# Kernel tuning notes

Measured on AMD Instinct MI355X. Metric: run time of the kernel, lower is better.

The kernel has to match this reference:

```python
import jax, jax.numpy as jnp
import numpy as np

B, S, H, NH = 2, 2048, 2048, 32
HD = H // NH  # 64

def _causal_mask(b, s, dtype=jnp.float32):
    neg = jnp.finfo(dtype).min
    m = jnp.where(jnp.tril(jnp.ones((s, s), dtype=bool)), 0.0, neg).astype(dtype)
    return jnp.broadcast_to(m[None, None], (b, 1, s, s))

def setup_inputs() -> dict:
    key = jax.random.key(0)
    k1, k2, k3, k4, k5 = jax.random.split(key, 5)
    scale = 1.0 / np.sqrt(H)
    return {
        "hidden_states": jax.random.normal(k1, (B, S, H), jnp.float32),
        "attention_mask": _causal_mask(B, S),
        "Wq": jax.random.normal(k2, (H, H), jnp.float32) * scale,
        "Wk": jax.random.normal(k3, (H, H), jnp.float32) * scale,
        "Wv": jax.random.normal(k4, (H, H), jnp.float32) * scale,
        "Wo": jax.random.normal(k5, (H, H), jnp.float32) * scale,
    }

def reference(hidden_states, attention_mask, Wq, Wk, Wv, Wo):
    b, s, _ = hidden_states.shape
    dt = hidden_states.dtype
    def proj(W):  # torch Linear: x @ W.T -> [b, nh, s, hd]
        return (hidden_states @ W.T).reshape(b, s, NH, HD).transpose(0, 2, 1, 3)
    q, k, v = proj(Wq), proj(Wk), proj(Wv)
    attn = jnp.einsum('bhqd,bhkd->bhqk', q, k) / np.sqrt(HD)
    attn = attn + attention_mask
    attn = jnp.maximum(attn, jnp.finfo(attn.dtype).min)
    attn = jax.nn.softmax(attn.astype(jnp.float32), axis=-1).astype(dt)
    out = jnp.einsum('bhqk,bhkd->bhqd', attn, v)
    out = out.transpose(0, 2, 1, 3).reshape(b, s, H)
    return out @ Wo.T
```

## Files before the change

### kernel.cpp

```cpp
#include <hip/hip_runtime.h>
#include <hip/hip_bf16.h>
#include <stdint.h>

#define S_LEN 2048
#define NHEAD 32
#define HDIM  64

using bf16x8 = __attribute__((ext_vector_type(8))) short;
using f32x4  = __attribute__((ext_vector_type(4))) float;

__device__ __forceinline__ uint16_t f2bf(float f) {
  union { float f; uint32_t u; } c; c.f = f;
  uint32_t u = c.u;
  return (uint16_t)((u + 0x7FFFu + ((u >> 16) & 1u)) >> 16);
}

__device__ __forceinline__ void load_lds16(const void* g, void* l) {
  __builtin_amdgcn_global_load_lds(
      (const __attribute__((address_space(1))) void*)g,
      (__attribute__((address_space(3))) void*)l, 16, 0, 0);
}

__global__ __launch_bounds__(256) void conv_f32_bf16(
    const float* __restrict__ in, uint16_t* __restrict__ out, int n4) {
  int i = blockIdx.x * 256 + threadIdx.x;
  if (i < n4) {
    float4 v = ((const float4*)in)[i];
    uint16_t o0 = f2bf(v.x), o1 = f2bf(v.y), o2 = f2bf(v.z), o3 = f2bf(v.w);
    uint64_t packed = (uint64_t)o0 | ((uint64_t)o1 << 16) |
                      ((uint64_t)o2 << 32) | ((uint64_t)o3 << 48);
    ((uint64_t*)out)[i] = packed;
  }
}

__global__ __launch_bounds__(512, 2) void gemm_qk(
    const uint16_t* __restrict__ A, const uint16_t* __restrict__ Bw,
    uint16_t* __restrict__ Qo, uint16_t* __restrict__ Ko, float qscale) {
  extern __shared__ char smem[];
  const int t = threadIdx.x;
  const int lane = t & 63, w = t >> 6;
  const int lrow = lane & 15, lgrp = lane >> 4;
  const int wr = w >> 2, wc = w & 3;
  const int id = blockIdx.x;
  const int swz = (id & 7) * 32 + (id >> 3);
  const int bm = (swz & 15) * 256, bn = (swz >> 4) * 256;
  constexpr int NT = 2048 / 32;

  const f32x4 zero4 = {0.f, 0.f, 0.f, 0.f};
  f32x4 acc[8][4];
#pragma unroll
  for (int mi = 0; mi < 8; ++mi)
#pragma unroll
    for (int ni = 0; ni < 4; ++ni) acc[mi][ni] = zero4;

  auto stage_mat = [&](const uint16_t* __restrict__ G, int grow0,
                       char* ldsbase, int kt) {
#pragma unroll
    for (int j = 0; j < 2; ++j) {
      const int s = t + j * 512;
      const int row = s >> 2;
      const int sc = (s & 3) ^ ((row >> 1) & 3);
      load_lds16(G + (size_t)(grow0 + row) * 2048 + kt + sc * 8,
                 ldsbase + j * 8192 + w * 1024);
    }
  };
  auto lda = [&](const char* Ab, int mi) -> bf16x8 {
    const int row = wr * 128 + mi * 16 + lrow;
    return *(const bf16x8*)(Ab + row * 64 + ((lgrp ^ ((row >> 1) & 3)) << 4));
  };
  auto ldb = [&](const char* Bb, int ni) -> bf16x8 {
    const int row = wc * 64 + ni * 16 + lrow;
    return *(const bf16x8*)(Bb + row * 64 + ((lgrp ^ ((row >> 1) & 3)) << 4));
  };

  stage_mat(A, bm, smem, 0);
  stage_mat(Bw, bn, smem + 16384, 0);
  stage_mat(A, bm, smem + 32768, 32);
  stage_mat(Bw, bn, smem + 32768 + 16384, 32);
  asm volatile("s_waitcnt vmcnt(4)" ::: "memory");
  __builtin_amdgcn_s_barrier();

  for (int kt = 0; kt < NT; ++kt) {
    char* cur = smem + (kt % 3) * 32768;
    char* nx2 = smem + ((kt + 2) % 3) * 32768;
    const int kg = (kt + 2) * 32;
    bf16x8 aF[4], bF[4];

    if (kt + 2 < NT) stage_mat(A, bm, nx2, kg);
#pragma unroll
    for (int mi = 0; mi < 4; ++mi) aF[mi] = lda(cur, mi);
#pragma unroll
    for (int ni = 0; ni < 4; ++ni) bF[ni] = ldb(cur + 16384, ni);
    __builtin_amdgcn_s_barrier();
    asm volatile("s_waitcnt lgkmcnt(0)" ::: "memory");
    __builtin_amdgcn_sched_barrier(0);
    __builtin_amdgcn_s_setprio(1);
#pragma unroll
    for (int mi = 0; mi < 4; ++mi)
#pragma unroll
      for (int ni = 0; ni < 4; ++ni)
        acc[mi][ni] = __builtin_amdgcn_mfma_f32_16x16x32_bf16(
            aF[mi], bF[ni], acc[mi][ni], 0, 0, 0);
    __builtin_amdgcn_s_setprio(0);
    __builtin_amdgcn_s_barrier();

    if (kt + 2 < NT) stage_mat(Bw, bn, nx2 + 16384, kg);
#pragma unroll
    for (int mi = 0; mi < 4; ++mi) aF[mi] = lda(cur, 4 + mi);
    __builtin_amdgcn_s_barrier();
    asm volatile("s_waitcnt lgkmcnt(0)" ::: "memory");
    __builtin_amdgcn_sched_barrier(0);
    __builtin_amdgcn_s_setprio(1);
#pragma unroll
    for (int mi = 0; mi < 4; ++mi)
#pragma unroll
      for (int ni = 0; ni < 4; ++ni)
        acc[4 + mi][ni] = __builtin_amdgcn_mfma_f32_16x16x32_bf16(
            aF[mi], bF[ni], acc[4 + mi][ni], 0, 0, 0);
    __builtin_amdgcn_s_setprio(0);
    if (kt < NT - 2) {
      asm volatile("s_waitcnt vmcnt(4)" ::: "memory");
    } else {
      asm volatile("s_waitcnt vmcnt(0)" ::: "memory");
    }
    __builtin_amdgcn_s_barrier();
  }

  const bool isQ = (bn < 2048);
#pragma unroll
  for (int mi = 0; mi < 8; ++mi) {
#pragma unroll
    for (int ni = 0; ni < 4; ++ni) {
      const int n = bn + wc * 64 + ni * 16 + lrow;
      const int n2 = isQ ? n : (n - 2048);
      const int h = n2 >> 6, d = n2 & 63;
#pragma unroll
      for (int r = 0; r < 4; ++r) {
        const int m = bm + wr * 128 + mi * 16 + lgrp * 4 + r;
        const int b = m >> 11, s = m & 2047;
        const size_t off = (((size_t)(b * NHEAD + h) * S_LEN + s) * HDIM) + d;
        if (isQ) Qo[off] = f2bf(acc[mi][ni][r] * qscale);
        else     Ko[off] = f2bf(acc[mi][ni][r]);
      }
    }
  }
}

template<int MODE>
__global__ __launch_bounds__(256) void gemm_nt(
    const uint16_t* __restrict__ A, const uint16_t* __restrict__ B,
    void* __restrict__ C, int M, int N, int K, float scale) {
  constexpr int BK = 64;
  __shared__ __align__(16) uint16_t As[128 * BK];
  __shared__ __align__(16) uint16_t Bs[128 * BK];

  const int t = threadIdx.x;
  const int lane = t & 63, w = t >> 6;
  const int lrow = lane & 15, lgrp = lane >> 4;
  const int bm = blockIdx.y * 128, bn = blockIdx.x * 128;
  const int wm = (w >> 1) * 64, wn = (w & 1) * 64;

  const f32x4 zero4 = {0.f, 0.f, 0.f, 0.f};
  f32x4 acc[4][4];
#pragma unroll
  for (int mi = 0; mi < 4; ++mi)
#pragma unroll
    for (int ni = 0; ni < 4; ++ni) acc[mi][ni] = zero4;

  const int rowS = t >> 3;
  const int chunk = t & 7;
  const int srcChunk = chunk ^ (rowS & 7);

  for (int kt = 0; kt < K; kt += BK) {
    __syncthreads();
#pragma unroll
    for (int it = 0; it < 4; ++it) {
      const int r = it * 32 + rowS;
      load_lds16(A + (size_t)(bm + r) * K + kt + srcChunk * 8,
                 (char*)As + it * 4096 + w * 1024);
      load_lds16(B + (size_t)(bn + r) * K + kt + srcChunk * 8,
                 (char*)Bs + it * 4096 + w * 1024);
    }
    __syncthreads();

#pragma unroll
    for (int ks = 0; ks < 2; ++ks) {
      bf16x8 af[4], bf[4];
#pragma unroll
      for (int mi = 0; mi < 4; ++mi) {
        const int ra = wm + mi * 16 + lrow;
        const int cb = ks * 4 + lgrp;
        af[mi] = *(const bf16x8*)((const char*)As +
                                  ra * 128 + ((cb ^ (ra & 7)) * 16));
        const int rb = wn + mi * 16 + lrow;
        bf[mi] = *(const bf16x8*)((const char*)Bs +
                                  rb * 128 + ((cb ^ (rb & 7)) * 16));
      }
#pragma unroll
      for (int mi = 0; mi < 4; ++mi)
#pragma unroll
        for (int ni = 0; ni < 4; ++ni)
          acc[mi][ni] = __builtin_amdgcn_mfma_f32_16x16x32_bf16(
              af[mi], bf[ni], acc[mi][ni], 0, 0, 0);
    }
  }

#pragma unroll
  for (int mi = 0; mi < 4; ++mi) {
#pragma unroll
    for (int ni = 0; ni < 4; ++ni) {
      const int n = bn + wn + ni * 16 + lrow;
#pragma unroll
      for (int r = 0; r < 4; ++r) {
        const int m = bm + wm + mi * 16 + lgrp * 4 + r;
        const float v = acc[mi][ni][r] * scale;
        if (MODE == 2) {
          ((float*)C)[(size_t)m * N + n] = v;
        } else {
          const int h = m >> 6, d = m & 63;
          const int b = n >> 11, s = n & 2047;
          ((uint16_t*)C)[(((size_t)(b * NHEAD + h) * HDIM + d) * S_LEN) + s] =
              f2bf(v);
        }
      }
    }
  }
}

__global__ __launch_bounds__(256, 4) void attn_kernel(
    const uint16_t* __restrict__ Q, const uint16_t* __restrict__ K,
    const uint16_t* __restrict__ Vt, uint16_t* __restrict__ O) {
  __shared__ __align__(16) uint16_t Ks[2][64 * 64];
  __shared__ __align__(16) uint16_t Vs[2][64 * 64];
  __shared__ __align__(16) uint16_t Ps[4][16 * 64];

  const int t = threadIdx.x, lane = t & 63, w = t >> 6;
  const int lrow = lane & 15, lgrp = lane >> 4;
  const int id = blockIdx.x;
  const int bh = (id & 7) | (((id >> 3) & 7) << 3);
  const int pair = id >> 6;
  const int b = bh >> 5, h = bh & 31;

  const uint16_t* Qbh = Q + (size_t)bh * S_LEN * HDIM;
  const uint16_t* Kbh = K + (size_t)bh * S_LEN * HDIM;
  const uint16_t* Vbh = Vt + (size_t)bh * HDIM * S_LEN;

  const int srow = lane >> 3;
  const int schunk = (lane & 7) ^ srow;

  const f32x4 zero4 = {0.f, 0.f, 0.f, 0.f};
  const int xk = lrow & 7;

  auto stage = [&](int k0, int bi) {
#pragma unroll
    for (int i = 0; i < 2; ++i) {
      const int r = i * 32 + w * 8 + srow;
      load_lds16(Kbh + (size_t)(k0 + r) * HDIM + schunk * 8,
                 (char*)&Ks[bi][0] + i * 4096 + w * 1024);
      load_lds16(Vbh + (size_t)r * S_LEN + k0 + schunk * 8,
                 (char*)&Vs[bi][0] + i * 4096 + w * 1024);
    }
  };

  for (int pass = 0; pass < 2; ++pass) {
    const int qt = pass ? (31 - pair) : pair;
    const int qbase = qt * 64 + w * 16;

    bf16x8 qf0, qf1;
    {
      const uint16_t* qp = Qbh + (size_t)(qbase + lrow) * HDIM + lgrp * 8;
      qf0 = *(const bf16x8*)qp;
      qf1 = *(const bf16x8*)(qp + 32);
    }
    f32x4 oacc[4] = {zero4, zero4, zero4, zero4};
    float lsum[4] = {0.f, 0.f, 0.f, 0.f};

    auto pstore = [&](int tt, int r, float p) {
      const int q = lgrp * 4 + r;
      const int c = (2 * tt + (lrow >> 3)) ^ (q & 7);
      Ps[w][q * 64 + c * 8 + (lrow & 7)] = f2bf(p);
    };

    for (int kt = 0; kt <= qt; ++kt) {
      const int cur = kt & 1;
      if (kt == 0) {
        __syncthreads();
        stage(0, 0);
      }
      __syncthreads();
      if (kt < qt) stage((kt + 1) * 64, cur ^ 1);

      const char* Kc = (const char*)&Ks[cur][0];
      const char* Vc = (const char*)&Vs[cur][0];
      const int k0 = kt * 64;

      auto qk_chunk = [&](int tt) -> f32x4 {
        const char* base = Kc + (tt * 16 + lrow) * 128;
        bf16x8 kf0 = *(const bf16x8*)(base + ((lgrp ^ xk) << 4));
        bf16x8 kf1 = *(const bf16x8*)(base + (((4 + lgrp) ^ xk) << 4));
        f32x4 s = __builtin_amdgcn_mfma_f32_16x16x32_bf16(qf0, kf0, zero4, 0, 0, 0);
        return __builtin_amdgcn_mfma_f32_16x16x32_bf16(qf1, kf1, s, 0, 0, 0);
      };

      if (kt < qt) {
        f32x4 sacc[4];
        __builtin_amdgcn_s_setprio(1);
#pragma unroll
        for (int tt = 0; tt < 4; ++tt) sacc[tt] = qk_chunk(tt);
        __builtin_amdgcn_s_setprio(0);
#pragma unroll
        for (int tt = 0; tt < 4; ++tt)
#pragma unroll
          for (int r = 0; r < 4; ++r) {
            const float p = __expf(sacc[tt][r]);
            lsum[r] += p;
            pstore(tt, r, p);
          }
      } else {
        for (int tt = 0; tt < 4; ++tt) {
          if (tt <= w) {
            const f32x4 s = qk_chunk(tt);
            const int kk = k0 + tt * 16 + lrow;
#pragma unroll
            for (int r = 0; r < 4; ++r) {
              const int qg = qbase + lgrp * 4 + r;
              const float p = (kk <= qg) ? __expf(s[r]) : 0.f;
              lsum[r] += p;
              pstore(tt, r, p);
            }
          } else {
#pragma unroll
            for (int r = 0; r < 4; ++r) pstore(tt, r, 0.f);
          }
        }
      }

      __builtin_amdgcn_s_setprio(1);
#pragma unroll
      for (int s = 0; s < 2; ++s) {
        const int cs = ((s << 2) + lgrp) ^ xk;
        bf16x8 pf = *(const bf16x8*)((const char*)&Ps[w][0] +
                                     lrow * 128 + (cs << 4));
#pragma unroll
        for (int dt = 0; dt < 4; ++dt) {
          bf16x8 vf = *(const bf16x8*)(Vc + (dt * 16 + lrow) * 128 + (cs << 4));
          oacc[dt] = __builtin_amdgcn_mfma_f32_16x16x32_bf16(pf, vf, oacc[dt],
                                                             0, 0, 0);
        }
      }
      __builtin_amdgcn_s_setprio(0);
    }

#pragma unroll
    for (int off = 1; off <= 8; off <<= 1)
#pragma unroll
      for (int r = 0; r < 4; ++r) lsum[r] += __shfl_xor(lsum[r], off, 64);

#pragma unroll
    for (int r = 0; r < 4; ++r) {
      const float inv = 1.0f / lsum[r];
      const int qg = qbase + lgrp * 4 + r;
#pragma unroll
      for (int dt = 0; dt < 4; ++dt)
        O[((size_t)b * S_LEN + qg) * 2048 + h * 64 + dt * 16 + lrow] =
            f2bf(oacc[dt][r] * inv);
    }
  }
}

extern "C" void kernel_launch(void* const* d_in, const int* in_sizes, int n_in,
                              void* d_out, int out_size, void* d_ws,
                              size_t ws_size, hipStream_t stream) {
  const float* X  = (const float*)d_in[0];
  const float* Wq = (const float*)d_in[2];
  const float* Wk = (const float*)d_in[3];
  const float* Wv = (const float*)d_in[4];
  const float* Wo = (const float*)d_in[5];
  float* out = (float*)d_out;

  char* ws = (char*)d_ws;
  uint16_t* Xbf = (uint16_t*)ws;
  uint16_t* Wqk = (uint16_t*)(ws + 16777216);
  uint16_t* Qb  = (uint16_t*)(ws + 33554432);
  uint16_t* Kb  = (uint16_t*)(ws + 50331648);
  uint16_t* Wsm = (uint16_t*)(ws + 67108864);
  uint16_t* Vtb = Wqk;
  uint16_t* Ob  = Xbf;

  const float qscale = 0.125f;

  hipFuncSetAttribute((const void*)gemm_qk,
                      hipFuncAttributeMaxDynamicSharedMemorySize, 98304);

  conv_f32_bf16<<<8192, 256, 0, stream>>>(X, Xbf, 2097152);
  conv_f32_bf16<<<4096, 256, 0, stream>>>(Wq, Wqk, 1048576);
  conv_f32_bf16<<<4096, 256, 0, stream>>>(Wk, Wqk + 4194304, 1048576);
  gemm_qk<<<256, 512, 98304, stream>>>(Xbf, Wqk, Qb, Kb, qscale);
  conv_f32_bf16<<<4096, 256, 0, stream>>>(Wv, Wsm, 1048576);
  gemm_nt<1><<<dim3(32, 16), 256, 0, stream>>>(Wsm, Xbf, Vtb, 2048, 4096, 2048, 1.0f);
  attn_kernel<<<dim3(1024), 256, 0, stream>>>(Qb, Kb, Vtb, Ob);
  conv_f32_bf16<<<4096, 256, 0, stream>>>(Wo, Wsm, 1048576);
  gemm_nt<2><<<dim3(16, 32), 256, 0, stream>>>(Ob, Wsm, out, 4096, 2048, 2048, 1.0f);
}
```

Before: 246.6 us.

## Rewrite attention with 32x32 MFMA, register-resident P, and batch input conversions

The attention kernel now gives each wave 32 query rows and uses 32x32x16 bf16 MFMAs. The S^T layout lets exponentiated scores be packed with v_cvt_pk_bf16_f32 and permlane32 swaps straight into A-operands, so the per-wave LDS round trip for P goes away. The grid is halved to 128-row query tiles with causal pairing and the occupancy hint drops to 3 blocks per SM. The X/Wq/Wk/Wv f32-to-bf16 conversions are merged into one launch, adding branchy source selection per thread and more register pressure in attention.

```diff
diff --git a/kernel.cpp b/kernel.cpp
--- a/kernel.cpp
+++ b/kernel.cpp
@@ -8,6 +8,7 @@
 
 using bf16x8 = __attribute__((ext_vector_type(8))) short;
 using f32x4  = __attribute__((ext_vector_type(4))) float;
+using f32x16 = __attribute__((ext_vector_type(16))) float;
 
 __device__ __forceinline__ uint16_t f2bf(float f) {
   union { float f; uint32_t u; } c; c.f = f;
@@ -19,6 +20,36 @@
   __builtin_amdgcn_global_load_lds(
       (const __attribute__((address_space(1))) void*)g,
       (__attribute__((address_space(3))) void*)l, 16, 0, 0);
+}
+
+__device__ __forceinline__ f32x16 mfma32(bf16x8 a, bf16x8 b, f32x16 c) {
+  return __builtin_amdgcn_mfma_f32_32x32x16_bf16(a, b, c, 0, 0, 0);
+}
+
+__device__ __forceinline__ uint32_t cvtpk(float lo, float hi_) {
+  uint32_t d;
+  asm("v_cvt_pk_bf16_f32 %0, %1, %2" : "=v"(d) : "v"(lo), "v"(hi_));
+  return d;
+}
+__device__ __forceinline__ void plswap(uint32_t& a, uint32_t& b) {
+  asm volatile("v_permlane32_swap_b32 %0, %1" : "+v"(a), "+v"(b));
+}
+
+__global__ __launch_bounds__(256) void conv_batch(
+    const float* __restrict__ X, const float* __restrict__ Wq,
+    const float* __restrict__ Wk, const float* __restrict__ Wv,
+    uint16_t* __restrict__ Xbf, uint16_t* __restrict__ Wqk,
+    uint16_t* __restrict__ Wvb) {
+  int i = blockIdx.x * 256 + threadIdx.x;
+  const float* src; uint16_t* dst; int o;
+  if (i < 2097152)      { src = X;  dst = Xbf;           o = i; }
+  else if (i < 3145728) { src = Wq; dst = Wqk;           o = i - 2097152; }
+  else if (i < 4194304) { src = Wk; dst = Wqk + 4194304; o = i - 3145728; }
+  else                  { src = Wv; dst = Wvb;           o = i - 4194304; }
+  float4 v = ((const float4*)src)[o];
+  uint64_t packed = (uint64_t)f2bf(v.x) | ((uint64_t)f2bf(v.y) << 16) |
+                    ((uint64_t)f2bf(v.z) << 32) | ((uint64_t)f2bf(v.w) << 48);
+  ((uint64_t*)dst)[o] = packed;
 }
 
 __global__ __launch_bounds__(256) void conv_f32_bf16(
@@ -26,9 +57,8 @@
   int i = blockIdx.x * 256 + threadIdx.x;
   if (i < n4) {
     float4 v = ((const float4*)in)[i];
-    uint16_t o0 = f2bf(v.x), o1 = f2bf(v.y), o2 = f2bf(v.z), o3 = f2bf(v.w);
-    uint64_t packed = (uint64_t)o0 | ((uint64_t)o1 << 16) |
-                      ((uint64_t)o2 << 32) | ((uint64_t)o3 << 48);
+    uint64_t packed = (uint64_t)f2bf(v.x) | ((uint64_t)f2bf(v.y) << 16) |
+                      ((uint64_t)f2bf(v.z) << 32) | ((uint64_t)f2bf(v.w) << 48);
     ((uint64_t*)out)[i] = packed;
   }
 }
@@ -227,18 +257,18 @@
   }
 }
 
-__global__ __launch_bounds__(256, 4) void attn_kernel(
+__global__ __launch_bounds__(256, 3) void attn_kernel(
     const uint16_t* __restrict__ Q, const uint16_t* __restrict__ K,
     const uint16_t* __restrict__ Vt, uint16_t* __restrict__ O) {
   __shared__ __align__(16) uint16_t Ks[2][64 * 64];
   __shared__ __align__(16) uint16_t Vs[2][64 * 64];
-  __shared__ __align__(16) uint16_t Ps[4][16 * 64];
+  __shared__ float Ls[4][32];
 
   const int t = threadIdx.x, lane = t & 63, w = t >> 6;
-  const int lrow = lane & 15, lgrp = lane >> 4;
+  const int qcol = lane & 31, hi = lane >> 5;
   const int id = blockIdx.x;
-  const int bh = (id & 7) | (((id >> 3) & 7) << 3);
-  const int pair = id >> 6;
+  const int bh = (id & 7) * 8 + ((id >> 3) & 7);
+  const int p = id >> 6;
   const int b = bh >> 5, h = bh & 31;
 
   const uint16_t* Qbh = Q + (size_t)bh * S_LEN * HDIM;
@@ -248,122 +278,124 @@
   const int srow = lane >> 3;
   const int schunk = (lane & 7) ^ srow;
 
-  const f32x4 zero4 = {0.f, 0.f, 0.f, 0.f};
-  const int xk = lrow & 7;
-
   auto stage = [&](int k0, int bi) {
 #pragma unroll
-    for (int i = 0; i < 2; ++i) {
-      const int r = i * 32 + w * 8 + srow;
+    for (int j = 0; j < 2; ++j) {
+      const int r = j * 32 + w * 8 + srow;
       load_lds16(Kbh + (size_t)(k0 + r) * HDIM + schunk * 8,
-                 (char*)&Ks[bi][0] + i * 4096 + w * 1024);
+                 (char*)&Ks[bi][0] + j * 4096 + w * 1024);
       load_lds16(Vbh + (size_t)r * S_LEN + k0 + schunk * 8,
-                 (char*)&Vs[bi][0] + i * 4096 + w * 1024);
+                 (char*)&Vs[bi][0] + j * 4096 + w * 1024);
     }
   };
 
   for (int pass = 0; pass < 2; ++pass) {
-    const int qt = pass ? (31 - pair) : pair;
-    const int qbase = qt * 64 + w * 16;
-
-    bf16x8 qf0, qf1;
+    const int jq = pass ? (15 - p) : p;
+    const int qw = jq * 128 + w * 32;
+    const int qg = qw + qcol;
+
+    bf16x8 qB[4];
     {
-      const uint16_t* qp = Qbh + (size_t)(qbase + lrow) * HDIM + lgrp * 8;
-      qf0 = *(const bf16x8*)qp;
-      qf1 = *(const bf16x8*)(qp + 32);
-    }
-    f32x4 oacc[4] = {zero4, zero4, zero4, zero4};
-    float lsum[4] = {0.f, 0.f, 0.f, 0.f};
-
-    auto pstore = [&](int tt, int r, float p) {
-      const int q = lgrp * 4 + r;
-      const int c = (2 * tt + (lrow >> 3)) ^ (q & 7);
-      Ps[w][q * 64 + c * 8 + (lrow & 7)] = f2bf(p);
-    };
-
-    for (int kt = 0; kt <= qt; ++kt) {
+      const uint16_t* qp = Qbh + (size_t)(qw + qcol) * HDIM + hi * 8;
+#pragma unroll
+      for (int j = 0; j < 4; ++j) qB[j] = *(const bf16x8*)(qp + 16 * j);
+    }
+
+    f32x16 oacc0, oacc1;
+#pragma unroll
+    for (int r = 0; r < 16; ++r) { oacc0[r] = 0.f; oacc1[r] = 0.f; }
+    float lsum = 0.f;
+
+    const int nt = 2 * jq + 2;
+    for (int kt = 0; kt < nt; ++kt) {
       const int cur = kt & 1;
-      if (kt == 0) {
-        __syncthreads();
-        stage(0, 0);
-      }
+      const int k0 = kt * 64;
+      if (kt == 0) { __syncthreads(); stage(0, 0); }
       __syncthreads();
-      if (kt < qt) stage((kt + 1) * 64, cur ^ 1);
-
-      const char* Kc = (const char*)&Ks[cur][0];
-      const char* Vc = (const char*)&Vs[cur][0];
-      const int k0 = kt * 64;
-
-      auto qk_chunk = [&](int tt) -> f32x4 {
-        const char* base = Kc + (tt * 16 + lrow) * 128;
-        bf16x8 kf0 = *(const bf16x8*)(base + ((lgrp ^ xk) << 4));
-        bf16x8 kf1 = *(const bf16x8*)(base + (((4 + lgrp) ^ xk) << 4));
-        f32x4 s = __builtin_amdgcn_mfma_f32_16x16x32_bf16(qf0, kf0, zero4, 0, 0, 0);
-        return __builtin_amdgcn_mfma_f32_16x16x32_bf16(qf1, kf1, s, 0, 0, 0);
-      };
-
-      if (kt < qt) {
-        f32x4 sacc[4];
+      if (kt + 1 < nt) stage((kt + 1) * 64, cur ^ 1);
+
+      if (k0 <= qw + 31) {
+        const char* Kc = (const char*)&Ks[cur][0];
+        const char* Vc = (const char*)&Vs[cur][0];
+
+        f32x16 s0, s1;
+#pragma unroll
+        for (int r = 0; r < 16; ++r) { s0[r] = 0.f; s1[r] = 0.f; }
+        const int rk0 = qcol, rk1 = 32 + qcol;
+        const int x0 = rk0 & 7;
         __builtin_amdgcn_s_setprio(1);
 #pragma unroll
-        for (int tt = 0; tt < 4; ++tt) sacc[tt] = qk_chunk(tt);
+        for (int j = 0; j < 4; ++j) {
+          bf16x8 kf0 = *(const bf16x8*)(Kc + rk0 * 128 + (((2*j+hi) ^ x0) << 4));
+          bf16x8 kf1 = *(const bf16x8*)(Kc + rk1 * 128 + (((2*j+hi) ^ x0) << 4));
+          s0 = mfma32(kf0, qB[j], s0);
+          s1 = mfma32(kf1, qB[j], s1);
+        }
         __builtin_amdgcn_s_setprio(0);
-#pragma unroll
-        for (int tt = 0; tt < 4; ++tt)
-#pragma unroll
-          for (int r = 0; r < 4; ++r) {
-            const float p = __expf(sacc[tt][r]);
-            lsum[r] += p;
-            pstore(tt, r, p);
+
+        if (k0 + 63 > qw) {
+#pragma unroll
+          for (int r = 0; r < 16; ++r) {
+            const int krow = (r & 3) + 8 * (r >> 2) + 4 * hi;
+            s0[r] = (k0 + krow <= qg) ? __expf(s0[r]) : 0.f;
+            s1[r] = (k0 + 32 + krow <= qg) ? __expf(s1[r]) : 0.f;
+            lsum += s0[r] + s1[r];
           }
-      } else {
-        for (int tt = 0; tt < 4; ++tt) {
-          if (tt <= w) {
-            const f32x4 s = qk_chunk(tt);
-            const int kk = k0 + tt * 16 + lrow;
-#pragma unroll
-            for (int r = 0; r < 4; ++r) {
-              const int qg = qbase + lgrp * 4 + r;
-              const float p = (kk <= qg) ? __expf(s[r]) : 0.f;
-              lsum[r] += p;
-              pstore(tt, r, p);
-            }
-          } else {
-#pragma unroll
-            for (int r = 0; r < 4; ++r) pstore(tt, r, 0.f);
+        } else {
+#pragma unroll
+          for (int r = 0; r < 16; ++r) {
+            s0[r] = __expf(s0[r]);
+            s1[r] = __expf(s1[r]);
+            lsum += s0[r] + s1[r];
           }
         }
+
+        bf16x8 paf[4];
+#pragma unroll
+        for (int tt = 0; tt < 4; ++tt) {
+          const int o = 8 * (tt & 1);
+          uint32_t a0, a1, a2, a3;
+          if (tt < 2) {
+            a0 = cvtpk(s0[o + 0], s0[o + 1]);
+            a1 = cvtpk(s0[o + 2], s0[o + 3]);
+            a2 = cvtpk(s0[o + 4], s0[o + 5]);
+            a3 = cvtpk(s0[o + 6], s0[o + 7]);
+          } else {
+            a0 = cvtpk(s1[o + 0], s1[o + 1]);
+            a1 = cvtpk(s1[o + 2], s1[o + 3]);
+            a2 = cvtpk(s1[o + 4], s1[o + 5]);
+            a3 = cvtpk(s1[o + 6], s1[o + 7]);
+          }
+          plswap(a0, a2);
+          plswap(a1, a3);
+          union { uint32_t u[4]; bf16x8 v; } pk;
+          pk.u[0] = a0; pk.u[1] = a1; pk.u[2] = a2; pk.u[3] = a3;
+          paf[tt] = pk.v;
+        }
+
+        __builtin_amdgcn_s_setprio(1);
+#pragma unroll
+        for (int tt = 0; tt < 4; ++tt) {
+          const int c = 2 * tt + hi;
+          bf16x8 v0f = *(const bf16x8*)(Vc + rk0 * 128 + ((c ^ x0) << 4));
+          bf16x8 v1f = *(const bf16x8*)(Vc + rk1 * 128 + ((c ^ x0) << 4));
+          oacc0 = mfma32(paf[tt], v0f, oacc0);
+          oacc1 = mfma32(paf[tt], v1f, oacc1);
+        }
+        __builtin_amdgcn_s_setprio(0);
       }
-
-      __builtin_amdgcn_s_setprio(1);
-#pragma unroll
-      for (int s = 0; s < 2; ++s) {
-        const int cs = ((s << 2) + lgrp) ^ xk;
-        bf16x8 pf = *(const bf16x8*)((const char*)&Ps[w][0] +
-                                     lrow * 128 + (cs << 4));
-#pragma unroll
-        for (int dt = 0; dt < 4; ++dt) {
-          bf16x8 vf = *(const bf16x8*)(Vc + (dt * 16 + lrow) * 128 + (cs << 4));
-          oacc[dt] = __builtin_amdgcn_mfma_f32_16x16x32_bf16(pf, vf, oacc[dt],
-                                                             0, 0, 0);
-        }
-      }
-      __builtin_amdgcn_s_setprio(0);
-    }
-
-#pragma unroll
-    for (int off = 1; off <= 8; off <<= 1)
-#pragma unroll
-      for (int r = 0; r < 4; ++r) lsum[r] += __shfl_xor(lsum[r], off, 64);
-
-#pragma unroll
-    for (int r = 0; r < 4; ++r) {
-      const float inv = 1.0f / lsum[r];
-      const int qg = qbase + lgrp * 4 + r;
-#pragma unroll
-      for (int dt = 0; dt < 4; ++dt)
-        O[((size_t)b * S_LEN + qg) * 2048 + h * 64 + dt * 16 + lrow] =
-            f2bf(oacc[dt][r] * inv);
+    }
+
+    lsum += __shfl_xor(lsum, 32, 64);
+    if (hi == 0) Ls[w][qcol] = 1.0f / lsum;
+
+#pragma unroll
+    for (int r = 0; r < 16; ++r) {
+      const int qrow = (r & 3) + 8 * (r >> 2) + 4 * hi;
+      const float inv = Ls[w][qrow];
+      const size_t base = ((size_t)b * S_LEN + qw + qrow) * 2048 + h * 64;
+      O[base + qcol] = f2bf(oacc0[r] * inv);
+      O[base + 32 + qcol] = f2bf(oacc1[r] * inv);
     }
   }
 }
@@ -392,13 +424,10 @@
   hipFuncSetAttribute((const void*)gemm_qk,
                       hipFuncAttributeMaxDynamicSharedMemorySize, 98304);
 
-  conv_f32_bf16<<<8192, 256, 0, stream>>>(X, Xbf, 2097152);
-  conv_f32_bf16<<<4096, 256, 0, stream>>>(Wq, Wqk, 1048576);
-  conv_f32_bf16<<<4096, 256, 0, stream>>>(Wk, Wqk + 4194304, 1048576);
+  conv_batch<<<20480, 256, 0, stream>>>(X, Wq, Wk, Wv, Xbf, Wqk, Wsm);
   gemm_qk<<<256, 512, 98304, stream>>>(Xbf, Wqk, Qb, Kb, qscale);
-  conv_f32_bf16<<<4096, 256, 0, stream>>>(Wv, Wsm, 1048576);
   gemm_nt<1><<<dim3(32, 16), 256, 0, stream>>>(Wsm, Xbf, Vtb, 2048, 4096, 2048, 1.0f);
-  attn_kernel<<<dim3(1024), 256, 0, stream>>>(Qb, Kb, Vtb, Ob);
+  attn_kernel<<<dim3(512), 256, 0, stream>>>(Qb, Kb, Vtb, Ob);
   conv_f32_bf16<<<4096, 256, 0, stream>>>(Wo, Wsm, 1048576);
   gemm_nt<2><<<dim3(16, 32), 256, 0, stream>>>(Ob, Wsm, out, 4096, 2048, 2048, 1.0f);
 }
```

Measured after the change: 234.2 us. -5.0%, faster.
